# Optimization experiments

Measured on AMD Instinct MI355X. Metric: run time of the kernel, lower is better.

Reference implementation:

```python
import jax, jax.numpy as jnp
import numpy as np

DIM = 256
NUM_HEADS = 8

def setup_inputs() -> dict:
    key = jax.random.key(0)
    ks = jax.random.split(key, 5)
    x = jax.random.normal(ks[0], (2, 4096, DIM), dtype=jnp.float32)
    s = 1.0 / np.sqrt(DIM)
    W_qkv = jax.random.normal(ks[1], (DIM, 3 * DIM), dtype=jnp.float32) * s
    b_qkv = jax.random.normal(ks[2], (3 * DIM,), dtype=jnp.float32) * 0.02
    W_proj = jax.random.normal(ks[3], (DIM, DIM), dtype=jnp.float32) * s
    b_proj = jax.random.normal(ks[4], (DIM,), dtype=jnp.float32) * 0.02
    return {"x": x, "W_qkv": W_qkv, "b_qkv": b_qkv, "W_proj": W_proj, "b_proj": b_proj}

def reference(x, W_qkv, b_qkv, W_proj, b_proj):
    B, N, C = x.shape
    H = NUM_HEADS
    Dh = C // H
    scale = C ** (-0.5)  # NOTE: original scales by full dim, not head_dim
    qkv = (x @ W_qkv + b_qkv).reshape(B, N, 3, H, Dh)
    q, k, v = jnp.moveaxis(qkv, 2, 0)  # each [B, N, H, Dh]
    q = q.transpose(0, 2, 1, 3)  # [B, H, N, Dh]
    k = k.transpose(0, 2, 1, 3)
    v = v.transpose(0, 2, 1, 3)
    attn = jnp.einsum('bhnd,bhmd->bhnm', q, k) * scale
    attn = jax.nn.softmax(attn, axis=-1)
    out = jnp.einsum('bhnm,bhmd->bhnd', attn, v)
    out = out.transpose(0, 2, 1, 3).reshape(B, N, C)
    return out @ W_proj + b_proj
```

## Files before the change

### kernel.cpp

```cpp
#include <hip/hip_runtime.h>

#define NSEQ 4096
#define BATCH 2
#define ROWS (BATCH * NSEQ)
#define NH 8
#define DHD 32

typedef __attribute__((ext_vector_type(8))) short bf16x8;
typedef __attribute__((ext_vector_type(4))) float f32x4;

static __device__ __forceinline__ ushort f2bf(float f) {
    union { float f; uint u; } v; v.f = f;
    uint u = v.u;
    uint r = (u + 0x7fffu + ((u >> 16) & 1u)) >> 16;
    return (ushort)r;
}

__global__ __launch_bounds__(256) void k_prep(const float* __restrict__ x,
                                              ushort* __restrict__ xb,
                                              const float* __restrict__ wqkv,
                                              const float* __restrict__ wproj,
                                              ushort* __restrict__ wqkvT,
                                              ushort* __restrict__ wprojT) {
    __shared__ float tile[32][33];
    int bid = blockIdx.x;
    if (bid < 2048) {
        int i = (bid * 256 + threadIdx.x) * 4;
        float4 v = *(const float4*)(x + i);
        ushort4 o;
        o.x = f2bf(v.x); o.y = f2bf(v.y); o.z = f2bf(v.z); o.w = f2bf(v.w);
        *(ushort4*)(xb + i) = o;
        return;
    }
    int tb = bid - 2048;
    int nt = tb & 31, kt = tb >> 5;
    const float* src; ushort* dst; int ncols, nbase;
    if (nt < 24) { src = wqkv;  dst = wqkvT;  ncols = 768; nbase = nt * 32; }
    else         { src = wproj; dst = wprojT; ncols = 256; nbase = (nt - 24) * 32; }
    int tx = threadIdx.x & 31, ty = threadIdx.x >> 5;
#pragma unroll
    for (int j = 0; j < 4; ++j)
        tile[ty + j * 8][tx] = src[(size_t)(kt * 32 + ty + j * 8) * ncols + nbase + tx];
    __syncthreads();
#pragma unroll
    for (int j = 0; j < 4; ++j)
        dst[(size_t)(nbase + ty + j * 8) * 256 + kt * 32 + tx] = f2bf(tile[tx][ty + j * 8]);
}

__global__ __launch_bounds__(256) void k_qkv(const ushort* __restrict__ xb,
                                             const ushort* __restrict__ wt,
                                             const float* __restrict__ bias,
                                             ushort* __restrict__ qh,
                                             ushort* __restrict__ kh,
                                             ushort* __restrict__ vT) {
    __shared__ __align__(16) ushort Al[64][264];
    __shared__ __align__(16) ushort Bl[64][264];
    int t = threadIdx.x;
    int w = t >> 6, lane = t & 63;
    int lhi = lane >> 4, llo = lane & 15;
    int row0 = blockIdx.x * 64;
    int n0 = blockIdx.y * 64;

#pragma unroll
    for (int j = 0; j < 8; ++j) {
        int f = j * 256 + t;
        int r = f >> 5, c = (f & 31) * 8;
        *(bf16x8*)&Al[r][c] = *(const bf16x8*)(xb + (size_t)(row0 + r) * 256 + c);
        *(bf16x8*)&Bl[r][c] = *(const bf16x8*)(wt + (size_t)(n0 + r) * 256 + c);
    }
    __syncthreads();

    f32x4 acc[4] = {};
#pragma unroll
    for (int ks = 0; ks < 8; ++ks) {
        int k0 = ks * 32 + lhi * 8;
        bf16x8 a = *(const bf16x8*)&Al[w * 16 + llo][k0];
#pragma unroll
        for (int fn = 0; fn < 4; ++fn) {
            bf16x8 b = *(const bf16x8*)&Bl[fn * 16 + llo][k0];
            acc[fn] = __builtin_amdgcn_mfma_f32_16x16x32_bf16(a, b, acc[fn], 0, 0, 0);
        }
    }

    int bb = row0 >> 12;
    int nb = row0 & 4095;
    if (blockIdx.y < 8) {
#pragma unroll
        for (int fn = 0; fn < 4; ++fn) {
            int cg = n0 + fn * 16 + llo;
            int three = cg >> 8, rem = cg & 255;
            int hh = rem >> 5, dh = rem & 31;
            float bv = bias[cg];
            size_t hb = (size_t)(bb * NH + hh);
#pragma unroll
            for (int r = 0; r < 4; ++r) {
                int n = nb + w * 16 + lhi * 4 + r;
                float v = acc[fn][r] + bv;
                if (three == 0) qh[(hb * 4096 + (size_t)n) * 32 + dh] = f2bf(v * 0.0625f);
                else            kh[(hb * 4096 + (size_t)n) * 32 + dh] = f2bf(v);
            }
        }
    } else {
        __syncthreads();
        ushort (*vbuf)[68] = (ushort(*)[68])&Al[0][0];
#pragma unroll
        for (int fn = 0; fn < 4; ++fn) {
            int c = fn * 16 + llo;
            float bv = bias[n0 + c];
#pragma unroll
            for (int r = 0; r < 4; ++r) {
                int s = w * 16 + lhi * 4 + r;
                int np = ((s >> 5) << 5) | (((s & 15) >> 2) << 3)
                       | (((s >> 4) & 1) << 2) | (s & 3);
                vbuf[c][np] = f2bf(acc[fn][r] + bv);
            }
        }
        __syncthreads();
#pragma unroll
        for (int j = 0; j < 2; ++j) {
            int f = j * 256 + t;
            int col = f >> 3, ch = (f & 7) * 8;
            bf16x8 val = *(const bf16x8*)&vbuf[col][ch];
            int dh = col & 31;
            int hh = ((int)blockIdx.y - 8) * 2 + (col >> 5);
            size_t hb = (size_t)(bb * NH + hh);
            *(bf16x8*)(vT + (hb * DHD + dh) * NSEQ + nb + ch) = val;
        }
    }
}

__global__ __launch_bounds__(256) void k_attn(const ushort* __restrict__ qh,
                                              const ushort* __restrict__ kh,
                                              const ushort* __restrict__ vT,
                                              ushort* __restrict__ attn_out) {
    __shared__ __align__(16) ushort Klds[2][64][40];
    __shared__ __align__(16) ushort Vlds[2][32][72];
    int t = threadIdx.x;
    int w = t >> 6, lane = t & 63;
    int lhi = lane >> 4, llo = lane & 15;
    int xcd = blockIdx.x & 7, qp = blockIdx.x >> 3;
    int bh = xcd * 2 + (qp >> 6);
    int qblk = qp & 63;
    int b = bh >> 3, h = bh & 7;
    int q0 = qblk * 64 + w * 16;

    const ushort* qbase = qh + (size_t)bh * 4096 * 32;
    const ushort* kg = kh + (size_t)bh * 4096 * 32 + (t >> 2) * 32 + (t & 3) * 8;
    const ushort* vg = vT + (size_t)bh * 32 * 4096 + (t >> 3) * 4096 + (t & 7) * 8;
    ushort* klp = &Klds[0][t >> 2][(t & 3) * 8];
    ushort* vlp = &Vlds[0][t >> 3][(t & 7) * 8];
    const int KLB = 64 * 40, VLB = 32 * 72;

    bf16x8 qf = *(const bf16x8*)(qbase + (q0 + llo) * 32 + lhi * 8);
    short onebits = (llo == 0) ? (short)0x3F80 : (short)0;
    bf16x8 va2 = {onebits, onebits, onebits, onebits, onebits, onebits, onebits, onebits};

    f32x4 acc0 = {}, acc1 = {}, acc2 = {};
    const float L2E = 1.4426950408889634f;
    float mrun = 0.f, nmL2E = 0.f, mthr = 8.f;
    const f32x4 zf = {0.f, 0.f, 0.f, 0.f};

    auto COMPUTE = [&](int cur) {
        const ushort* Kb = &Klds[cur][0][0];
        const ushort* Vb = &Vlds[cur][0][0];
        bf16x8 k0 = *(const bf16x8*)(Kb + (llo) * 40 + lhi * 8);
        bf16x8 k1 = *(const bf16x8*)(Kb + (16 + llo) * 40 + lhi * 8);
        bf16x8 k2 = *(const bf16x8*)(Kb + (32 + llo) * 40 + lhi * 8);
        bf16x8 k3 = *(const bf16x8*)(Kb + (48 + llo) * 40 + lhi * 8);
        bf16x8 v00 = *(const bf16x8*)(Vb + llo * 72 + lhi * 8);
        bf16x8 v01 = *(const bf16x8*)(Vb + (llo + 16) * 72 + lhi * 8);
        bf16x8 v10 = *(const bf16x8*)(Vb + llo * 72 + 32 + lhi * 8);
        bf16x8 v11 = *(const bf16x8*)(Vb + (llo + 16) * 72 + 32 + lhi * 8);
        __builtin_amdgcn_s_setprio(1);
        f32x4 sf0 = __builtin_amdgcn_mfma_f32_16x16x32_bf16(k0, qf, zf, 0, 0, 0);
        f32x4 sf1 = __builtin_amdgcn_mfma_f32_16x16x32_bf16(k1, qf, zf, 0, 0, 0);
        f32x4 sf2 = __builtin_amdgcn_mfma_f32_16x16x32_bf16(k2, qf, zf, 0, 0, 0);
        f32x4 sf3 = __builtin_amdgcn_mfma_f32_16x16x32_bf16(k3, qf, zf, 0, 0, 0);
        __builtin_amdgcn_s_setprio(0);
        float g0 = fmaxf(fmaxf(sf0[0], sf0[1]), sf0[2]);
        float g1 = fmaxf(fmaxf(sf0[3], sf1[0]), sf1[1]);
        float g2 = fmaxf(fmaxf(sf1[2], sf1[3]), sf2[0]);
        float g3 = fmaxf(fmaxf(sf2[1], sf2[2]), sf2[3]);
        float g4 = fmaxf(fmaxf(sf3[0], sf3[1]), sf3[2]);
        float h0 = fmaxf(fmaxf(g0, g1), g2);
        float h1 = fmaxf(fmaxf(g3, g4), sf3[3]);
        float tm = fmaxf(h0, h1);
        if (!__all(tm <= mthr)) {
            float rmax = fmaxf(tm, __shfl_xor(tm, 16));
            rmax = fmaxf(rmax, __shfl_xor(rmax, 32));
            float mnew = fmaxf(mrun, rmax);
            float corr = __builtin_amdgcn_exp2f((mrun - mnew) * L2E);
            mrun = mnew; nmL2E = -mrun * L2E; mthr = mrun + 8.f;
#pragma unroll
            for (int r = 0; r < 4; ++r) {
                float fc = __shfl(corr, lhi * 4 + r);
                acc0[r] *= fc; acc1[r] *= fc; acc2[r] *= fc;
            }
        }
        float e00 = __builtin_amdgcn_exp2f(__builtin_fmaf(sf0[0], L2E, nmL2E));
        float e01 = __builtin_amdgcn_exp2f(__builtin_fmaf(sf0[1], L2E, nmL2E));
        float e02 = __builtin_amdgcn_exp2f(__builtin_fmaf(sf0[2], L2E, nmL2E));
        float e03 = __builtin_amdgcn_exp2f(__builtin_fmaf(sf0[3], L2E, nmL2E));
        float e10 = __builtin_amdgcn_exp2f(__builtin_fmaf(sf1[0], L2E, nmL2E));
        float e11 = __builtin_amdgcn_exp2f(__builtin_fmaf(sf1[1], L2E, nmL2E));
        float e12 = __builtin_amdgcn_exp2f(__builtin_fmaf(sf1[2], L2E, nmL2E));
        float e13 = __builtin_amdgcn_exp2f(__builtin_fmaf(sf1[3], L2E, nmL2E));
        float e20 = __builtin_amdgcn_exp2f(__builtin_fmaf(sf2[0], L2E, nmL2E));
        float e21 = __builtin_amdgcn_exp2f(__builtin_fmaf(sf2[1], L2E, nmL2E));
        float e22 = __builtin_amdgcn_exp2f(__builtin_fmaf(sf2[2], L2E, nmL2E));
        float e23 = __builtin_amdgcn_exp2f(__builtin_fmaf(sf2[3], L2E, nmL2E));
        float e30 = __builtin_amdgcn_exp2f(__builtin_fmaf(sf3[0], L2E, nmL2E));
        float e31 = __builtin_amdgcn_exp2f(__builtin_fmaf(sf3[1], L2E, nmL2E));
        float e32 = __builtin_amdgcn_exp2f(__builtin_fmaf(sf3[2], L2E, nmL2E));
        float e33 = __builtin_amdgcn_exp2f(__builtin_fmaf(sf3[3], L2E, nmL2E));
        union PU { uint u[4]; bf16x8 v; };
        PU pa0, pa1;
        asm("v_cvt_pk_bf16_f32 %0, %1, %2" : "=v"(pa0.u[0]) : "v"(e00), "v"(e01));
        asm("v_cvt_pk_bf16_f32 %0, %1, %2" : "=v"(pa0.u[1]) : "v"(e02), "v"(e03));
        asm("v_cvt_pk_bf16_f32 %0, %1, %2" : "=v"(pa0.u[2]) : "v"(e10), "v"(e11));
        asm("v_cvt_pk_bf16_f32 %0, %1, %2" : "=v"(pa0.u[3]) : "v"(e12), "v"(e13));
        asm("v_cvt_pk_bf16_f32 %0, %1, %2" : "=v"(pa1.u[0]) : "v"(e20), "v"(e21));
        asm("v_cvt_pk_bf16_f32 %0, %1, %2" : "=v"(pa1.u[1]) : "v"(e22), "v"(e23));
        asm("v_cvt_pk_bf16_f32 %0, %1, %2" : "=v"(pa1.u[2]) : "v"(e30), "v"(e31));
        asm("v_cvt_pk_bf16_f32 %0, %1, %2" : "=v"(pa1.u[3]) : "v"(e32), "v"(e33));
        __builtin_amdgcn_s_setprio(1);
        acc0 = __builtin_amdgcn_mfma_f32_16x16x32_bf16(pa0.v, v00, acc0, 0, 0, 0);
        acc1 = __builtin_amdgcn_mfma_f32_16x16x32_bf16(pa0.v, v01, acc1, 0, 0, 0);
        acc2 = __builtin_amdgcn_mfma_f32_16x16x32_bf16(pa0.v, va2, acc2, 0, 0, 0);
        acc0 = __builtin_amdgcn_mfma_f32_16x16x32_bf16(pa1.v, v10, acc0, 0, 0, 0);
        acc1 = __builtin_amdgcn_mfma_f32_16x16x32_bf16(pa1.v, v11, acc1, 0, 0, 0);
        acc2 = __builtin_amdgcn_mfma_f32_16x16x32_bf16(pa1.v, va2, acc2, 0, 0, 0);
        __builtin_amdgcn_s_setprio(0);
    };

    {
        bf16x8 ka = *(const bf16x8*)(kg);
        bf16x8 va = *(const bf16x8*)(vg);
        bf16x8 kb = *(const bf16x8*)(kg + 2048);
        bf16x8 vb = *(const bf16x8*)(vg + 64);
        *(bf16x8*)(klp) = ka;
        *(bf16x8*)(vlp) = va;
        *(bf16x8*)(klp + KLB) = kb;
        *(bf16x8*)(vlp + VLB) = vb;
    }
    __syncthreads();

#pragma unroll 1
    for (int it = 0; it < 32; ++it) {
        bf16x8 ksA, vsA, ksB, vsB;
        if (it + 1 < 32) {
            int tn = 2 * it + 2;
            ksA = *(const bf16x8*)(kg + (size_t)tn * 2048);
            vsA = *(const bf16x8*)(vg + tn * 64);
            ksB = *(const bf16x8*)(kg + (size_t)(tn + 1) * 2048);
            vsB = *(const bf16x8*)(vg + (tn + 1) * 64);
        }
        COMPUTE(0);
        COMPUTE(1);
        __syncthreads();
        if (it + 1 < 32) {
            *(bf16x8*)(klp) = ksA;
            *(bf16x8*)(vlp) = vsA;
            *(bf16x8*)(klp + KLB) = ksB;
            *(bf16x8*)(vlp + VLB) = vsB;
            __syncthreads();
        }
    }

#pragma unroll
    for (int r = 0; r < 4; ++r) {
        float ls = __shfl(acc2[r], lhi * 16);
        float li = 1.f / ls;
        int row = q0 + lhi * 4 + r;
        size_t orow = ((size_t)(b * NSEQ) + row) * 256 + h * DHD;
        attn_out[orow + llo] = f2bf(acc0[r] * li);
        attn_out[orow + 16 + llo] = f2bf(acc1[r] * li);
    }
}

__global__ __launch_bounds__(256) void k_proj(const ushort* __restrict__ aout,
                                              const ushort* __restrict__ wt,
                                              const float* __restrict__ bias,
                                              float* __restrict__ out) {
    __shared__ __align__(16) ushort Al[64][264];
    __shared__ __align__(16) ushort Bl[64][264];
    int t = threadIdx.x;
    int w = t >> 6, lane = t & 63;
    int lhi = lane >> 4, llo = lane & 15;
    int row0 = blockIdx.x * 64;
    int n0 = blockIdx.y * 64;

#pragma unroll
    for (int j = 0; j < 8; ++j) {
        int f = j * 256 + t;
        int r = f >> 5, c = (f & 31) * 8;
        *(bf16x8*)&Al[r][c] = *(const bf16x8*)(aout + (size_t)(row0 + r) * 256 + c);
        *(bf16x8*)&Bl[r][c] = *(const bf16x8*)(wt + (size_t)(n0 + r) * 256 + c);
    }
    __syncthreads();

    f32x4 acc[4] = {};
#pragma unroll
    for (int ks = 0; ks < 8; ++ks) {
        int k0 = ks * 32 + lhi * 8;
        bf16x8 a = *(const bf16x8*)&Al[w * 16 + llo][k0];
#pragma unroll
        for (int fn = 0; fn < 4; ++fn) {
            bf16x8 b = *(const bf16x8*)&Bl[fn * 16 + llo][k0];
            acc[fn] = __builtin_amdgcn_mfma_f32_16x16x32_bf16(a, b, acc[fn], 0, 0, 0);
        }
    }
#pragma unroll
    for (int fn = 0; fn < 4; ++fn) {
        int cg = n0 + fn * 16 + llo;
        float bv = bias[cg];
#pragma unroll
        for (int r = 0; r < 4; ++r) {
            int row = row0 + w * 16 + lhi * 4 + r;
            out[(size_t)row * 256 + cg] = acc[fn][r] + bv;
        }
    }
}

extern "C" void kernel_launch(void* const* d_in, const int* in_sizes, int n_in,
                              void* d_out, int out_size, void* d_ws, size_t ws_size,
                              hipStream_t stream) {
    const float* x     = (const float*)d_in[0];
    const float* Wqkv  = (const float*)d_in[1];
    const float* bqkv  = (const float*)d_in[2];
    const float* Wproj = (const float*)d_in[3];
    const float* bproj = (const float*)d_in[4];
    float* out = (float*)d_out;

    char* ws = (char*)d_ws;
    ushort* xb     = (ushort*)(ws);
    ushort* wqkvT  = (ushort*)(ws + 4194304);
    ushort* wprojT = (ushort*)(ws + 4587520);
    ushort* qhb    = (ushort*)(ws + 4718592);
    ushort* khb    = (ushort*)(ws + 8912896);
    ushort* vT     = (ushort*)(ws + 13107200);
    ushort* aoutb  = (ushort*)(ws + 17301504);

    k_prep<<<2304, 256, 0, stream>>>(x, xb, Wqkv, Wproj, wqkvT, wprojT);
    k_qkv<<<dim3(128, 12), 256, 0, stream>>>(xb, wqkvT, bqkv, qhb, khb, vT);
    k_attn<<<1024, 256, 0, stream>>>(qhb, khb, vT, aoutb);
    k_proj<<<dim3(128, 4), 256, 0, stream>>>(aoutb, wprojT, bproj, out);
}
```

Baseline: 96.41 us.

## Use four-stage LDS ring for K/V tiles to halve barriers

The attention kernel's K/V shared-memory staging grows from two to four tile slots and processes two tile-pairs per loop iteration. Writes into the idle half of the ring go ahead while the other half is being computed, which removes one of the two __syncthreads per pair of tiles. In exchange it doubles LDS usage per block, which may lower occupancy, and it raises register pressure from holding prefetched tiles across compute phases.

Result: faster. 94.15 us, median of 2 (-2.3%).

```diff
diff --git a/kernel.cpp b/kernel.cpp
--- a/kernel.cpp
+++ b/kernel.cpp
@@ -133,8 +133,8 @@
                                               const ushort* __restrict__ kh,
                                               const ushort* __restrict__ vT,
                                               ushort* __restrict__ attn_out) {
-    __shared__ __align__(16) ushort Klds[2][64][40];
-    __shared__ __align__(16) ushort Vlds[2][32][72];
+    __shared__ __align__(16) ushort Klds[4][64][40];
+    __shared__ __align__(16) ushort Vlds[4][32][72];
     int t = threadIdx.x;
     int w = t >> 6, lane = t & 63;
     int lhi = lane >> 4, llo = lane & 15;
@@ -234,37 +234,49 @@
     };
 
     {
-        bf16x8 ka = *(const bf16x8*)(kg);
-        bf16x8 va = *(const bf16x8*)(vg);
-        bf16x8 kb = *(const bf16x8*)(kg + 2048);
-        bf16x8 vb = *(const bf16x8*)(vg + 64);
-        *(bf16x8*)(klp) = ka;
-        *(bf16x8*)(vlp) = va;
-        *(bf16x8*)(klp + KLB) = kb;
-        *(bf16x8*)(vlp + VLB) = vb;
+        bf16x8 k0t = *(const bf16x8*)(kg);
+        bf16x8 v0t = *(const bf16x8*)(vg);
+        bf16x8 k1t = *(const bf16x8*)(kg + 2048);
+        bf16x8 v1t = *(const bf16x8*)(vg + 64);
+        *(bf16x8*)(klp) = k0t;
+        *(bf16x8*)(vlp) = v0t;
+        *(bf16x8*)(klp + KLB) = k1t;
+        *(bf16x8*)(vlp + VLB) = v1t;
     }
     __syncthreads();
+    bf16x8 kA = *(const bf16x8*)(kg + 2 * 2048);
+    bf16x8 vA = *(const bf16x8*)(vg + 2 * 64);
+    bf16x8 kB = *(const bf16x8*)(kg + 3 * 2048);
+    bf16x8 vB = *(const bf16x8*)(vg + 3 * 64);
 
 #pragma unroll 1
-    for (int it = 0; it < 32; ++it) {
-        bf16x8 ksA, vsA, ksB, vsB;
-        if (it + 1 < 32) {
-            int tn = 2 * it + 2;
-            ksA = *(const bf16x8*)(kg + (size_t)tn * 2048);
-            vsA = *(const bf16x8*)(vg + tn * 64);
-            ksB = *(const bf16x8*)(kg + (size_t)(tn + 1) * 2048);
-            vsB = *(const bf16x8*)(vg + (tn + 1) * 64);
+    for (int ip = 0; ip < 16; ++ip) {
+        *(bf16x8*)(klp + 2 * KLB) = kA;
+        *(bf16x8*)(vlp + 2 * VLB) = vA;
+        *(bf16x8*)(klp + 3 * KLB) = kB;
+        *(bf16x8*)(vlp + 3 * VLB) = vB;
+        if (ip < 15) {
+            kA = *(const bf16x8*)(kg + (size_t)(4 * ip + 4) * 2048);
+            vA = *(const bf16x8*)(vg + (4 * ip + 4) * 64);
+            kB = *(const bf16x8*)(kg + (size_t)(4 * ip + 5) * 2048);
+            vB = *(const bf16x8*)(vg + (4 * ip + 5) * 64);
         }
         COMPUTE(0);
         COMPUTE(1);
         __syncthreads();
-        if (it + 1 < 32) {
-            *(bf16x8*)(klp) = ksA;
-            *(bf16x8*)(vlp) = vsA;
-            *(bf16x8*)(klp + KLB) = ksB;
-            *(bf16x8*)(vlp + VLB) = vsB;
-            __syncthreads();
-        }
+        if (ip < 15) {
+            *(bf16x8*)(klp) = kA;
+            *(bf16x8*)(vlp) = vA;
+            *(bf16x8*)(klp + KLB) = kB;
+            *(bf16x8*)(vlp + VLB) = vB;
+            kA = *(const bf16x8*)(kg + (size_t)(4 * ip + 6) * 2048);
+            vA = *(const bf16x8*)(vg + (4 * ip + 6) * 64);
+            kB = *(const bf16x8*)(kg + (size_t)(4 * ip + 7) * 2048);
+            vB = *(const bf16x8*)(vg + (4 * ip + 7) * 64);
+        }
+        COMPUTE(2);
+        COMPUTE(3);
+        __syncthreads();
     }
 
 #pragma unroll
```
